# Kernel tuning notes

Measured on AMD Instinct MI355X. Metric: run time of the kernel, lower is better.

Reference implementation:

```python
import jax, jax.numpy as jnp
import numpy as np

SIGMA = 0.01        # config['fscore_sigma']
FSCORE_W = 0.1      # config['fscore_weight']
TASK_W = 1.0        # config['task_weight']
DOMAIN_W = 0.1      # config['domain_weight']


def setup_inputs() -> dict:
    key = jax.random.key(0)
    ks = jax.random.split(key, 11)
    B, N, M, F = 8, 4096, 4096, 512
    H1, H2, D = 256, 128, 6
    return {
        "pred_pc": jax.random.normal(ks[0], (B, N, 3), jnp.float32),
        "target_pc": jax.random.normal(ks[1], (B, M, 3), jnp.float32),
        "domain_features": jax.random.normal(ks[2], (B, F), jnp.float32),
        "dataset_weights": jax.random.uniform(ks[3], (B,), jnp.float32, 0.9, 1.2),
        "W1": jax.random.normal(ks[4], (F, H1), jnp.float32) * 0.02,
        "b1": jnp.zeros((H1,), jnp.float32),
        "W2": jax.random.normal(ks[5], (H1, H2), jnp.float32) * 0.02,
        "b2": jnp.zeros((H2,), jnp.float32),
        "W3": jax.random.normal(ks[6], (H2, D), jnp.float32) * 0.02,
        "b3": jnp.zeros((D,), jnp.float32),
        "domain_labels": jax.random.randint(ks[7], (B,), 0, D),
    }


def _chamfer_mins(pred, tgt):
    # pred: [B,N,3], tgt: [B,M,3] -> squared pairwise dists [B,N,M], then dual mins
    d = (jnp.sum(pred ** 2, axis=2)[:, :, None]
         + jnp.sum(tgt ** 2, axis=2)[:, None, :]
         - 2.0 * jnp.einsum('bnd,bmd->bnm', pred, tgt))
    return jnp.min(d, axis=2), jnp.min(d, axis=1)   # [B,N], [B,M]


def reference(pred_pc, target_pc, domain_features, dataset_weights,
              W1, b1, W2, b2, W3, b3, domain_labels):
    min_a, min_b = _chamfer_mins(pred_pc, target_pc)
    c = 2.0 * SIGMA * SIGMA
    soft_a = jnp.exp(-min_a / c)
    soft_b = jnp.exp(-min_b / c)

    # batch-level task loss (compute_reconstruction_loss on full batch)
    chamfer = jnp.mean(min_a) + jnp.mean(min_b)
    prec = jnp.mean(soft_a)
    rec = jnp.mean(soft_b)
    fscore = 2.0 * prec * rec / (prec + rec + 1e-8)
    task = chamfer + FSCORE_W * (1.0 - fscore)

    # per-sample dataset-weighted loss (vectorized form of the Python loop)
    ch_i = jnp.mean(min_a, axis=1) + jnp.mean(min_b, axis=1)
    p_i = jnp.mean(soft_a, axis=1)
    r_i = jnp.mean(soft_b, axis=1)
    f_i = 2.0 * p_i * r_i / (p_i + r_i + 1e-8)
    loss_i = ch_i + FSCORE_W * (1.0 - f_i)
    dataset_weighted = jnp.mean(dataset_weights * loss_i)

    # domain loss: GRL is identity in forward; classifier in eval mode (dropout off)
    h = jax.nn.relu(domain_features @ W1 + b1)
    h = jax.nn.relu(h @ W2 + b2)
    logits = h @ W3 + b3
    logp = jax.nn.log_softmax(logits, axis=-1)
    domain = -jnp.mean(jnp.take_along_axis(logp, domain_labels[:, None], axis=1))

    total = TASK_W * task + DOMAIN_W * domain + dataset_weighted
    return total
```

## Files before the change

kernel.cpp:

```cpp
#include <hip/hip_runtime.h>
#include <math.h>

#define B 8
#define NPTS 4096
#define SPLITS 32
#define LOG2S 5
#define REFS (NPTS / SPLITS)
#define QPT 8
#define THREADS 256


__device__ __forceinline__ void final_combine_atomic(
    float* sums32, float* nlls, const float* w, float* out) {
  float chamfer = 0.f, prec = 0.f, rec = 0.f, dsw = 0.f, dom = 0.f;
  for (int b = 0; b < B; ++b) {
    float sa  = atomicAdd(&sums32[(0 * B + b) * 2 + 0], 0.f);
    float ssa = atomicAdd(&sums32[(0 * B + b) * 2 + 1], 0.f);
    float sb  = atomicAdd(&sums32[(1 * B + b) * 2 + 0], 0.f);
    float ssb = atomicAdd(&sums32[(1 * B + b) * 2 + 1], 0.f);
    float nb  = atomicAdd(&nlls[b], 0.f);
    float ma = sa / 4096.f, mb = sb / 4096.f;
    float p = ssa / 4096.f, r = ssb / 4096.f;
    chamfer += ma + mb;
    prec += p; rec += r;
    float f_i = 2.f * p * r / (p + r + 1e-8f);
    float loss_i = ma + mb + 0.1f * (1.f - f_i);
    dsw += w[b] * loss_i;
    dom += nb;
  }
  chamfer *= (1.f / B); prec *= (1.f / B); rec *= (1.f / B);
  dsw *= (1.f / B); dom *= (1.f / B);
  float fscore = 2.f * prec * rec / (prec + rec + 1e-8f);
  float task = chamfer + 0.1f * (1.f - fscore);
  out[0] = 1.0f * task + 0.1f * dom + dsw;
}

__global__ __launch_bounds__(THREADS, 4) void k_main(
    const float* __restrict__ pred, const float* __restrict__ targ,
    const float* __restrict__ x, const float* __restrict__ W1,
    float* __restrict__ partial, float* __restrict__ sums32,
    float* __restrict__ h1p, unsigned int* __restrict__ cnt) {
  int id = blockIdx.x, tid = threadIdx.x;
  __shared__ float4 sbuf4[REFS];

  if (id >= 1024) {
    if (id == 1088) {
      if (tid < 32) sums32[tid] = 0.f;
      if (tid == 0) cnt[0] = 0u;
      return;
    }
    int lid = id - 1024;
    int b = lid >> 3, kc = lid & 7;
    float* xs = (float*)sbuf4;
    if (tid < 64) xs[tid] = x[b * 512 + kc * 64 + tid];
    __syncthreads();
    float acc = 0.f;
    const float* w = W1 + (size_t)(kc * 64) * 256 + tid;
#pragma unroll 8
    for (int k = 0; k < 64; ++k) acc = fmaf(xs[k], w[k * 256], acc);
    h1p[(b * 8 + kc) * 256 + tid] = acc;
    return;
  }

  int split  = id & (SPLITS - 1);
  int qchunk = (id >> LOG2S) & 1;
  int b      = (id >> (LOG2S + 1)) & 7;
  int dir    = id >> (LOG2S + 4);
  const float* qp = dir ? targ : pred;
  const float* rp = dir ? pred : targ;

  float4* refs = sbuf4;
  const float* rb = rp + ((size_t)b * NPTS + (size_t)split * REFS) * 3;
  for (int i = tid; i < REFS; i += THREADS) {
    float xx = rb[i * 3 + 0], yy = rb[i * 3 + 1], zz = rb[i * 3 + 2];
    refs[i] = make_float4(xx, yy, zz, 0.5f * (xx * xx + yy * yy + zz * zz));
  }
  __syncthreads();

  const float* qb = qp + (size_t)b * NPTS * 3;
  int q0 = qchunk * (QPT * THREADS) + tid;
  float qx[QPT], qy[QPT], qz[QPT], vmin[QPT];
#pragma unroll
  for (int i = 0; i < QPT; ++i) {
    int q = q0 + i * THREADS;
    qx[i] = qb[q * 3 + 0];
    qy[i] = qb[q * 3 + 1];
    qz[i] = qb[q * 3 + 2];
    vmin[i] = 3.4e38f;
  }

  for (int j = 0; j < REFS; j += 4) {
    float4 t0 = refs[j + 0], t1 = refs[j + 1];
    float4 t2 = refs[j + 2], t3 = refs[j + 3];
    asm volatile("" : "+v"(t0.x), "+v"(t0.y), "+v"(t0.z), "+v"(t0.w),
                      "+v"(t1.x), "+v"(t1.y), "+v"(t1.z), "+v"(t1.w),
                      "+v"(t2.x), "+v"(t2.y), "+v"(t2.z), "+v"(t2.w),
                      "+v"(t3.x), "+v"(t3.y), "+v"(t3.z), "+v"(t3.w));
#pragma unroll
    for (int i = 0; i < QPT; ++i) {
      float s0 = fmaf(-qx[i], t0.x, fmaf(-qy[i], t0.y, fmaf(-qz[i], t0.z, t0.w)));
      float s1 = fmaf(-qx[i], t1.x, fmaf(-qy[i], t1.y, fmaf(-qz[i], t1.z, t1.w)));
      float s2 = fmaf(-qx[i], t2.x, fmaf(-qy[i], t2.y, fmaf(-qz[i], t2.z, t2.w)));
      float s3 = fmaf(-qx[i], t3.x, fmaf(-qy[i], t3.y, fmaf(-qz[i], t3.z, t3.w)));
      vmin[i] = fminf(fminf(vmin[i], fminf(s0, s1)), fminf(s2, s3));
    }
  }

  size_t base = (((size_t)dir * B + b) * SPLITS + split) * NPTS;
#pragma unroll
  for (int i = 0; i < QPT; ++i) {
    float qn = fmaf(qx[i], qx[i], fmaf(qy[i], qy[i], qz[i] * qz[i]));
    partial[base + q0 + i * THREADS] = fmaf(2.f, vmin[i], qn);
  }
}

__global__ __launch_bounds__(THREADS) void k_finish(
    const float* __restrict__ partial, float* __restrict__ sums32,
    const float* __restrict__ h1p, const float* __restrict__ b1,
    const float* __restrict__ W2, const float* __restrict__ b2,
    const float* __restrict__ W3, const float* __restrict__ b3,
    const int* __restrict__ labels, const float* __restrict__ wgt,
    float* __restrict__ nlls, unsigned int* __restrict__ cnt,
    float* __restrict__ out) {
  int id = blockIdx.x, tid = threadIdx.x;
  __shared__ float sbuf[4160];
  __shared__ unsigned int sflag;

  if (id < 128) {
    int chunk = id & 7;
    int b   = (id >> 3) & 7;
    int dir = id >> 6;
    size_t pb = (size_t)(dir * B + b) * SPLITS * NPTS;
    float s_min = 0.f, s_soft = 0.f;
#pragma unroll
    for (int i = 0; i < 2; ++i) {
      int q = chunk * 512 + i * 256 + tid;
      float m = 3.4e38f;
#pragma unroll
      for (int s = 0; s < SPLITS; ++s)
        m = fminf(m, partial[pb + (size_t)s * NPTS + q]);
      s_min  += m;
      s_soft += __expf(-5000.0f * m);
    }
    for (int off = 32; off > 0; off >>= 1) {
      s_min  += __shfl_down(s_min,  off);
      s_soft += __shfl_down(s_soft, off);
    }
    int wave = tid >> 6, lane = tid & 63;
    if (lane == 0) { sbuf[wave * 2] = s_min; sbuf[wave * 2 + 1] = s_soft; }
    __syncthreads();
    if (tid == 0) {
      float a = 0.f, c = 0.f;
      for (int w = 0; w < 4; ++w) { a += sbuf[w * 2]; c += sbuf[w * 2 + 1]; }
      float o0 = atomicAdd(&sums32[(dir * B + b) * 2 + 0], a);
      float o1 = atomicAdd(&sums32[(dir * B + b) * 2 + 1], c);
      asm volatile("" :: "v"(o0), "v"(o1));
      unsigned int old = atomicAdd(cnt, 1u);
      sflag = (old == 128u) ? 1u : 0u;
    }
    __syncthreads();
    if (sflag && tid == 0) final_combine_atomic(sums32, nlls, wgt, out);
    return;
  }

  float* h1s = sbuf;
  float* pp  = sbuf + 2048;
  float* lg  = sbuf + 4096;
  for (int i = tid; i < 2048; i += THREADS) {
    int bb = i >> 8, j = i & 255;
    float a = b1[j];
#pragma unroll
    for (int kc = 0; kc < 8; ++kc) a += h1p[(bb * 8 + kc) * 256 + j];
    h1s[i] = fmaxf(a, 0.f);
  }
  __syncthreads();
  {
    int j = tid & 127, half = tid >> 7;
    float acc[8];
#pragma unroll
    for (int bb = 0; bb < 8; ++bb) acc[bb] = 0.f;
    const float* w = W2 + (size_t)(half * 128) * 128 + j;
    for (int k = 0; k < 128; ++k) {
      float wv = w[k * 128];
      int kk = half * 128 + k;
#pragma unroll
      for (int bb = 0; bb < 8; ++bb)
        acc[bb] = fmaf(h1s[bb * 256 + kk], wv, acc[bb]);
    }
#pragma unroll
    for (int bb = 0; bb < 8; ++bb) pp[(half * 8 + bb) * 128 + j] = acc[bb];
  }
  __syncthreads();
  float* h2s = sbuf;
  for (int i = tid; i < 1024; i += THREADS) {
    int bb = i >> 7, j = i & 127;
    float a = b2[j] + pp[(0 * 8 + bb) * 128 + j] + pp[(1 * 8 + bb) * 128 + j];
    h2s[i] = fmaxf(a, 0.f);
  }
  __syncthreads();
  if (tid < 48) {
    int bb = tid / 6, d = tid % 6;
    float acc = b3[d];
#pragma unroll 8
    for (int k = 0; k < 128; ++k) acc = fmaf(h2s[bb * 128 + k], W3[k * 6 + d], acc);
    lg[tid] = acc;
  }
  __syncthreads();
  if (tid < 8) {
    int bb = tid;
    float mx = lg[bb * 6];
    for (int d = 1; d < 6; ++d) mx = fmaxf(mx, lg[bb * 6 + d]);
    float se = 0.f;
    for (int d = 0; d < 6; ++d) se += __expf(lg[bb * 6 + d] - mx);
    int lab = labels[bb];
    float old = atomicExch(&nlls[bb], -(lg[bb * 6 + lab] - mx - __logf(se)));
    asm volatile("" :: "v"(old));
  }
  __syncthreads();
  if (tid == 0) {
    unsigned int old = atomicAdd(cnt, 1u);
    sflag = (old == 128u) ? 1u : 0u;
  }
  __syncthreads();
  if (sflag && tid == 0) final_combine_atomic(sums32, nlls, wgt, out);
}

extern "C" void kernel_launch(void* const* d_in, const int* in_sizes, int n_in,
                              void* d_out, int out_size, void* d_ws, size_t ws_size,
                              hipStream_t stream) {
  const float* pred   = (const float*)d_in[0];
  const float* targ   = (const float*)d_in[1];
  const float* x      = (const float*)d_in[2];
  const float* wgt    = (const float*)d_in[3];
  const float* W1     = (const float*)d_in[4];
  const float* b1     = (const float*)d_in[5];
  const float* W2     = (const float*)d_in[6];
  const float* b2     = (const float*)d_in[7];
  const float* W3     = (const float*)d_in[8];
  const float* b3     = (const float*)d_in[9];
  const int*   labels = (const int*)d_in[10];
  float* out = (float*)d_out;
  char* ws = (char*)d_ws;

  float* partial = (float*)ws;
  float* sums32  = partial + (size_t)2 * B * SPLITS * NPTS;
  float* h1p     = sums32 + 32;
  float* nlls    = h1p + 64 * 256;
  unsigned int* cnt = (unsigned int*)(nlls + 8);

  hipLaunchKernelGGL(k_main, dim3(1089), dim3(THREADS), 0, stream,
                     pred, targ, x, W1, partial, sums32, h1p, cnt);
  hipLaunchKernelGGL(k_finish, dim3(129), dim3(THREADS), 0, stream,
                     partial, sums32, h1p, b1, W2, b2, W3, b3, labels, wgt,
                     nlls, cnt, out);
}
```

Measured before the change: 126.9 us.

## Prefetch next ref tile into registers and vectorize partial-min reduction

The chamfer inner loop now loads the next four reference float4s from shared memory while the current four are being used, a register double buffer meant to hide LDS latency behind the FMA/min work. The finish kernel's reduction over split partials now uses float4 loads with 64 blocks covering 1024 queries each, instead of 128 blocks using scalar loads. The last-block completion check and the grid size are updated to match. The changes add register pressure in the main loop and halve the number of reduction blocks, which may reduce memory parallelism.

```diff
diff --git a/kernel.cpp b/kernel.cpp
--- a/kernel.cpp
+++ b/kernel.cpp
@@ -89,13 +89,15 @@
     vmin[i] = 3.4e38f;
   }
 
+  float4 t0 = refs[0], t1 = refs[1], t2 = refs[2], t3 = refs[3];
+  asm volatile("" : "+v"(t0.x), "+v"(t0.y), "+v"(t0.z), "+v"(t0.w),
+                    "+v"(t1.x), "+v"(t1.y), "+v"(t1.z), "+v"(t1.w),
+                    "+v"(t2.x), "+v"(t2.y), "+v"(t2.z), "+v"(t2.w),
+                    "+v"(t3.x), "+v"(t3.y), "+v"(t3.z), "+v"(t3.w));
   for (int j = 0; j < REFS; j += 4) {
-    float4 t0 = refs[j + 0], t1 = refs[j + 1];
-    float4 t2 = refs[j + 2], t3 = refs[j + 3];
-    asm volatile("" : "+v"(t0.x), "+v"(t0.y), "+v"(t0.z), "+v"(t0.w),
-                      "+v"(t1.x), "+v"(t1.y), "+v"(t1.z), "+v"(t1.w),
-                      "+v"(t2.x), "+v"(t2.y), "+v"(t2.z), "+v"(t2.w),
-                      "+v"(t3.x), "+v"(t3.y), "+v"(t3.z), "+v"(t3.w));
+    int jn = (j + 4) & (REFS - 1);
+    float4 n0 = refs[jn + 0], n1 = refs[jn + 1];
+    float4 n2 = refs[jn + 2], n3 = refs[jn + 3];
 #pragma unroll
     for (int i = 0; i < QPT; ++i) {
       float s0 = fmaf(-qx[i], t0.x, fmaf(-qy[i], t0.y, fmaf(-qz[i], t0.z, t0.w)));
@@ -104,6 +106,11 @@
       float s3 = fmaf(-qx[i], t3.x, fmaf(-qy[i], t3.y, fmaf(-qz[i], t3.z, t3.w)));
       vmin[i] = fminf(fminf(vmin[i], fminf(s0, s1)), fminf(s2, s3));
     }
+    asm volatile("" : "+v"(n0.x), "+v"(n0.y), "+v"(n0.z), "+v"(n0.w),
+                      "+v"(n1.x), "+v"(n1.y), "+v"(n1.z), "+v"(n1.w),
+                      "+v"(n2.x), "+v"(n2.y), "+v"(n2.z), "+v"(n2.w),
+                      "+v"(n3.x), "+v"(n3.y), "+v"(n3.z), "+v"(n3.w));
+    t0 = n0; t1 = n1; t2 = n2; t3 = n3;
   }
 
   size_t base = (((size_t)dir * B + b) * SPLITS + split) * NPTS;
@@ -126,22 +133,21 @@
   __shared__ float sbuf[4160];
   __shared__ unsigned int sflag;
 
-  if (id < 128) {
-    int chunk = id & 7;
-    int b   = (id >> 3) & 7;
-    int dir = id >> 6;
-    size_t pb = (size_t)(dir * B + b) * SPLITS * NPTS;
-    float s_min = 0.f, s_soft = 0.f;
-#pragma unroll
-    for (int i = 0; i < 2; ++i) {
-      int q = chunk * 512 + i * 256 + tid;
-      float m = 3.4e38f;
-#pragma unroll
-      for (int s = 0; s < SPLITS; ++s)
-        m = fminf(m, partial[pb + (size_t)s * NPTS + q]);
-      s_min  += m;
-      s_soft += __expf(-5000.0f * m);
-    }
+  if (id < 64) {
+    int dirb  = id >> 2;
+    int chunk = id & 3;
+    const float* pbase = partial + (size_t)dirb * SPLITS * NPTS
+                       + (size_t)chunk * 1024 + (size_t)tid * 4;
+    float4 m4 = make_float4(3.4e38f, 3.4e38f, 3.4e38f, 3.4e38f);
+#pragma unroll
+    for (int s = 0; s < SPLITS; ++s) {
+      float4 v = *(const float4*)(pbase + (size_t)s * NPTS);
+      m4.x = fminf(m4.x, v.x); m4.y = fminf(m4.y, v.y);
+      m4.z = fminf(m4.z, v.z); m4.w = fminf(m4.w, v.w);
+    }
+    float s_min  = (m4.x + m4.y) + (m4.z + m4.w);
+    float s_soft = (__expf(-5000.0f * m4.x) + __expf(-5000.0f * m4.y))
+                 + (__expf(-5000.0f * m4.z) + __expf(-5000.0f * m4.w));
     for (int off = 32; off > 0; off >>= 1) {
       s_min  += __shfl_down(s_min,  off);
       s_soft += __shfl_down(s_soft, off);
@@ -152,11 +158,11 @@
     if (tid == 0) {
       float a = 0.f, c = 0.f;
       for (int w = 0; w < 4; ++w) { a += sbuf[w * 2]; c += sbuf[w * 2 + 1]; }
-      float o0 = atomicAdd(&sums32[(dir * B + b) * 2 + 0], a);
-      float o1 = atomicAdd(&sums32[(dir * B + b) * 2 + 1], c);
+      float o0 = atomicAdd(&sums32[dirb * 2 + 0], a);
+      float o1 = atomicAdd(&sums32[dirb * 2 + 1], c);
       asm volatile("" :: "v"(o0), "v"(o1));
       unsigned int old = atomicAdd(cnt, 1u);
-      sflag = (old == 128u) ? 1u : 0u;
+      sflag = (old == 64u) ? 1u : 0u;
     }
     __syncthreads();
     if (sflag && tid == 0) final_combine_atomic(sums32, nlls, wgt, out);
@@ -219,7 +225,7 @@
   __syncthreads();
   if (tid == 0) {
     unsigned int old = atomicAdd(cnt, 1u);
-    sflag = (old == 128u) ? 1u : 0u;
+    sflag = (old == 64u) ? 1u : 0u;
   }
   __syncthreads();
   if (sflag && tid == 0) final_combine_atomic(sums32, nlls, wgt, out);
@@ -250,7 +256,7 @@
 
   hipLaunchKernelGGL(k_main, dim3(1089), dim3(THREADS), 0, stream,
                      pred, targ, x, W1, partial, sums32, h1p, cnt);
-  hipLaunchKernelGGL(k_finish, dim3(129), dim3(THREADS), 0, stream,
+  hipLaunchKernelGGL(k_finish, dim3(65), dim3(THREADS), 0, stream,
                      partial, sums32, h1p, b1, W2, b2, W3, b3, labels, wgt,
                      nlls, cnt, out);
 }
```

After: 123.5 us. -2.7%, faster.
